# Kernel optimization log

Hardware: AMD Instinct MI355X
Metric: run time of the kernel (lower is better)

The kernel has to match this reference:

```python
import jax, jax.numpy as jnp
import numpy as np

NEG_INF = -1e9  # module uses -1e9 negativeInfinity constant
BS, DA, SL, H = 16, 512, 1024, 8


def setup_inputs() -> dict:
    key = jax.random.key(0)
    ks = jax.random.split(key, 8)
    return {
        "q":    jax.random.normal(ks[0], (BS, DA, SL), dtype=jnp.float32),
        "k_in": jax.random.normal(ks[1], (BS, DA, SL), dtype=jnp.float32),
        "v_in": jax.random.normal(ks[2], (BS, DA, SL), dtype=jnp.float32),
        "k_w":  jax.random.normal(ks[3], (DA, DA), dtype=jnp.float32) * 0.05,
        "k_b":  jax.random.normal(ks[4], (DA,), dtype=jnp.float32) * 0.05,
        "v_w":  jax.random.normal(ks[5], (DA, DA), dtype=jnp.float32) * 0.05,
        "v_b":  jax.random.normal(ks[6], (DA,), dtype=jnp.float32) * 0.05,
        "gbn_gamma": jnp.ones((H,), dtype=jnp.float32),
        "gbn_bias":  jnp.zeros((H,), dtype=jnp.float32),
        "gbn_m":     jnp.zeros((H,), dtype=jnp.float32),
        "gbn_s":     jnp.ones((H,), dtype=jnp.float32),
        "mask": jax.random.randint(ks[7], (BS, 1, 1, SL), 0, 2, dtype=jnp.int32),
    }


def reference(q, k_in, v_in, k_w, k_b, v_w, v_b, gbn_gamma, gbn_bias, gbn_m, gbn_s, mask):
    bs, da, qsl = q.shape
    h = gbn_gamma.shape[0]
    dh = da // h
    sl = k_in.shape[2]
    mask_b = mask.astype(bool)                 # [bs,1,1,sl] True = masked

    # 1x1 conv1d projections == per-position matmul over channels
    k = jnp.einsum('ok,bks->bos', k_w, k_in) + k_b[None, :, None]   # [bs,da,sl]
    v = jnp.einsum('ov,bvs->bos', v_w, v_in) + v_b[None, :, None]   # [bs,dva,sl]
    dva = v.shape[1]
    dvh = dva // h

    qh = q.reshape(bs, h, dh, qsl).transpose(0, 1, 3, 2)   # [bs,h,qsl,dh]
    kh = k.reshape(bs, h, dh, sl)                          # [bs,h,dh,sl]
    vh = v.reshape(bs, h, dvh, sl).transpose(0, 1, 3, 2)   # [bs,h,sl,dvh]

    scores = jnp.einsum('bhqd,bhds->bhqs', qh, kh)         # [bs,h,qsl,sl]

    # GhostBatchNorm1d(features=h) in eval mode: per-head affine normalization
    scores = (scores - gbn_m[None, :, None, None]) / gbn_s[None, :, None, None]
    scores = scores * gbn_gamma[None, :, None, None] + gbn_bias[None, :, None, None]

    mask_k = mask_b                           # [bs,1,1,sl]  mask key positions (selfAttention fill)
    mask_q = jnp.swapaxes(mask_b, 2, 3)       # [bs,1,sl,1]  mask query rows (transposed fill)
    scores = jnp.where(mask_k, NEG_INF, scores)
    scores = jnp.where(mask_q, NEG_INF, scores)

    w = jax.nn.softmax(scores, axis=-1)
    w = jnp.where(mask_q, 0.0, w)             # v_weights.masked_fill(mask, 0)

    out = jnp.einsum('bhqs,bhsd->bhqd', w, vh)             # [bs,h,qsl,dvh]
    out = out.transpose(0, 1, 3, 2).reshape(bs, dva, qsl)  # back to channels-first
    return out
```

## Files before the change

kernel.cpp:

```cpp
#include <hip/hip_runtime.h>

typedef _Float16 f16;
typedef _Float16 h8_t __attribute__((ext_vector_type(8)));
typedef _Float16 h4_t __attribute__((ext_vector_type(4)));
typedef float f32x4 __attribute__((ext_vector_type(4)));
typedef float f32x16 __attribute__((ext_vector_type(16)));

#define BS 16
#define DA 512
#define SL 1024
#define NH 8
#define DH 64

__device__ __forceinline__ void gload_lds16(const void* g, void* l) {
  __builtin_amdgcn_global_load_lds((const __attribute__((address_space(1))) void*)g,
                                   (__attribute__((address_space(3))) void*)l, 16, 0, 0);
}

__global__ __launch_bounds__(256) void prep_kernel(
    const float* __restrict__ k_in, const float* __restrict__ v_in,
    const float* __restrict__ k_w, const float* __restrict__ v_w,
    f16* __restrict__ Kt, f16* __restrict__ Vt,
    f16* __restrict__ kwh, f16* __restrict__ vwh) {
  const int blk = blockIdx.x;
  const int t = threadIdx.x;
  if (blk < 2048) {
    const int which = blk >> 10;
    const int r = blk & 1023;
    const int b = r >> 6;
    const int c0 = ((r >> 3) & 7) * 64;
    const int s0 = (r & 7) * 128;
    const float* src = which ? v_in : k_in;
    f16* dst = which ? Vt : Kt;
    __shared__ __align__(16) float Xf32[64 * 132];
#pragma unroll
    for (int p = 0; p < 8; ++p) {
      const int idx = p * 256 + t;
      const int cc = idx >> 5, s4 = (idx & 31) * 4;
      const float4 v = *(const float4*)&src[((size_t)b * DA + c0 + cc) * SL + s0 + s4];
      *(float4*)&Xf32[cc * 132 + s4] = v;
    }
    __syncthreads();
    const int srow = t >> 1, cb = (t & 1) * 32;
#pragma unroll
    for (int g = 0; g < 4; ++g) {
      h8_t h;
#pragma unroll
      for (int u = 0; u < 8; ++u) h[u] = (f16)Xf32[(cb + g * 8 + u) * 132 + srow];
      *(h8_t*)&dst[((size_t)b * SL + s0 + srow) * DA + c0 + cb + g * 8] = h;
    }
  } else {
    const int r = blk - 2048;
    const int wsel = r >> 5;
    const float* src = wsel ? v_w : k_w;
    f16* dst = wsel ? vwh : kwh;
    const int base = (r & 31) * 8192;
#pragma unroll
    for (int p = 0; p < 4; ++p) {
      const int i = base + p * 2048 + t * 8;
      const float4 a = *(const float4*)&src[i];
      const float4 c = *(const float4*)&src[i + 4];
      h8_t h;
      h[0] = (f16)a.x; h[1] = (f16)a.y; h[2] = (f16)a.z; h[3] = (f16)a.w;
      h[4] = (f16)c.x; h[5] = (f16)c.y; h[6] = (f16)c.z; h[7] = (f16)c.w;
      *(h8_t*)&dst[i] = h;
    }
  }
}

__global__ __launch_bounds__(256, 4) void proj_gemm_all(
    const f16* __restrict__ kwh, const f16* __restrict__ vwh,
    const f16* __restrict__ Kt, const f16* __restrict__ Vt,
    const float* __restrict__ k_b, const float* __restrict__ v_b,
    f16* __restrict__ kp, f16* __restrict__ vp) {
  __shared__ __align__(16) f16 LD[2][8192];
  const int mode = blockIdx.z;
  const int b = blockIdx.y;
  const int tx = blockIdx.x;
  const int m0 = (mode ? (tx >> 2) : (tx & 3)) * 128;
  const int n0 = (mode ? (tx & 3) : (tx >> 2)) * 128;
  const int t = threadIdx.x;
  const int lane = t & 63, w = t >> 6, lr = lane & 15, lq = lane >> 4;
  const int wm = (w >> 1) * 64, wn = (w & 1) * 64;

  const f16* Arow = (mode ? Vt + (size_t)b * SL * DA : kwh) + (size_t)m0 * DA;
  const f16* Brow = (mode ? vwh : Kt + (size_t)b * SL * DA) + (size_t)n0 * DA;

  const int rr = t >> 2;
  const int c8 = (t & 3) * 8;
  const int lo8 = t * 8;

  const f16* ga0 = Arow + (size_t)rr * DA + c8;
  const f16* ga1 = Arow + (size_t)(64 + rr) * DA + c8;
  const f16* gb0 = Brow + (size_t)rr * DA + c8;
  const f16* gb1 = Brow + (size_t)(64 + rr) * DA + c8;

  f32x4 acc[4][4] = {};

  gload_lds16(ga0, &LD[0][0] + lo8);
  gload_lds16(ga1, &LD[0][2048] + lo8);
  gload_lds16(gb0, &LD[0][4096] + lo8);
  gload_lds16(gb1, &LD[0][6144] + lo8);
  ga0 += 32; ga1 += 32; gb0 += 32; gb1 += 32;

  for (int kt = 0; kt < 16; ++kt) {
    const int cur = kt & 1;
    if (kt < 15) {
      f16* nb = &LD[cur ^ 1][0];
      gload_lds16(ga0, nb + lo8);
      gload_lds16(ga1, nb + 2048 + lo8);
      gload_lds16(gb0, nb + 4096 + lo8);
      gload_lds16(gb1, nb + 6144 + lo8);
      ga0 += 32; ga1 += 32; gb0 += 32; gb1 += 32;
      asm volatile("s_waitcnt vmcnt(4)" ::: "memory");
    } else {
      asm volatile("s_waitcnt vmcnt(0)" ::: "memory");
    }
    __builtin_amdgcn_s_barrier();
    __builtin_amdgcn_sched_barrier(0);

    const f16* Al = &LD[cur][0];
    const f16* Bl = &LD[cur][4096];
    h8_t af[4], bf[4];
#pragma unroll
    for (int i = 0; i < 4; ++i) af[i] = *(const h8_t*)&Al[(wm + i * 16 + lr) * 32 + lq * 8];
#pragma unroll
    for (int j = 0; j < 4; ++j) bf[j] = *(const h8_t*)&Bl[(wn + j * 16 + lr) * 32 + lq * 8];
    __builtin_amdgcn_s_setprio(1);
#pragma unroll
    for (int i = 0; i < 4; ++i)
#pragma unroll
      for (int j = 0; j < 4; ++j)
        acc[i][j] = __builtin_amdgcn_mfma_f32_16x16x32_f16(af[i], bf[j], acc[i][j], 0, 0, 0);
    __builtin_amdgcn_s_setprio(0);

    if (kt < 15) {
      __builtin_amdgcn_sched_barrier(0);
      __builtin_amdgcn_s_barrier();
      __builtin_amdgcn_sched_barrier(0);
    }
  }

#pragma unroll
  for (int i = 0; i < 4; ++i) {
    const int gmb = m0 + wm + i * 16 + lq * 4;
    float bm[4] = {0.f, 0.f, 0.f, 0.f};
    if (mode == 0) {
      const float4 b4 = *(const float4*)&k_b[gmb];
      bm[0] = b4.x; bm[1] = b4.y; bm[2] = b4.z; bm[3] = b4.w;
    }
#pragma unroll
    for (int j = 0; j < 4; ++j) {
      const int gn = n0 + wn + j * 16 + lr;
      const float bn = mode ? v_b[gn] : 0.f;
      h4_t hv;
#pragma unroll
      for (int r = 0; r < 4; ++r) {
        const float val = acc[i][j][r] + (mode == 0 ? bm[r] : bn);
        hv[r] = (f16)val;
      }
      f16* dst = mode ? &vp[((size_t)b * DA + gn) * SL + gmb]
                      : &kp[((size_t)b * SL + gn) * DA + gmb];
      *(h4_t*)dst = hv;
    }
  }
}

template <int MODE>
__global__ __launch_bounds__(256) void fused_proj(const float* __restrict__ Wg,
                                                  const float* __restrict__ Xin,
                                                  const float* __restrict__ bias,
                                                  f16* __restrict__ outg) {
  constexpr int MT = MODE ? SL : DA;
  constexpr int NT = MODE ? DA : SL;
  __shared__ f16 Wl[128 * 40];
  __shared__ f16 Xl[128 * 40];
  __shared__ float Xf32[32 * 132];
  const int b = blockIdx.z;
  const int m0 = blockIdx.x * 128;
  const int n0 = blockIdx.y * 128;
  const int o_base = MODE ? n0 : m0;
  const int s_base = MODE ? m0 : n0;
  const int t = threadIdx.x;
  const int w = t >> 6, lane = t & 63, lr = lane & 15, lq = lane >> 4;
  const int wm = (w >> 1) * 64, wn = (w & 1) * 64;

  f32x4 acc[4][4] = {};

  for (int kt = 0; kt < 16; ++kt) {
    const int c0 = kt * 32;
    __syncthreads();
#pragma unroll
    for (int p = 0; p < 4; ++p) {
      const int idx = p * 256 + t;
      const int row = idx >> 3, cq = (idx & 7) * 4;
      const float4 v = *(const float4*)&Wg[(size_t)(o_base + row) * DA + c0 + cq];
      h4_t hv;
      hv[0] = (f16)v.x; hv[1] = (f16)v.y; hv[2] = (f16)v.z; hv[3] = (f16)v.w;
      *(h4_t*)&Wl[row * 40 + cq] = hv;
    }
#pragma unroll
    for (int p = 0; p < 4; ++p) {
      const int idx = p * 256 + t;
      const int cc = idx >> 5, s4 = (idx & 31) * 4;
      const float4 v = *(const float4*)&Xin[((size_t)b * DA + c0 + cc) * SL + s_base + s4];
      *(float4*)&Xf32[cc * 132 + s4] = v;
    }
    __syncthreads();
    {
      const int srow = t >> 1, cb = (t & 1) * 16;
      h8_t lo, hi;
#pragma unroll
      for (int u = 0; u < 8; ++u) lo[u] = (f16)Xf32[(cb + u) * 132 + srow];
#pragma unroll
      for (int u = 0; u < 8; ++u) hi[u] = (f16)Xf32[(cb + 8 + u) * 132 + srow];
      *(h8_t*)&Xl[srow * 40 + cb] = lo;
      *(h8_t*)&Xl[srow * 40 + cb + 8] = hi;
    }
    __syncthreads();
    const f16* Alp = MODE ? Xl : Wl;
    const f16* Blp = MODE ? Wl : Xl;
    h8_t af[4], bf[4];
#pragma unroll
    for (int i = 0; i < 4; ++i) af[i] = *(const h8_t*)&Alp[(wm + i * 16 + lr) * 40 + lq * 8];
#pragma unroll
    for (int j = 0; j < 4; ++j) bf[j] = *(const h8_t*)&Blp[(wn + j * 16 + lr) * 40 + lq * 8];
#pragma unroll
    for (int i = 0; i < 4; ++i)
#pragma unroll
      for (int j = 0; j < 4; ++j)
        acc[i][j] = __builtin_amdgcn_mfma_f32_16x16x32_f16(af[i], bf[j], acc[i][j], 0, 0, 0);
  }

#pragma unroll
  for (int i = 0; i < 4; ++i) {
    const int gmb = m0 + wm + i * 16 + lq * 4;
    float bm[4] = {0.f, 0.f, 0.f, 0.f};
    if (MODE == 0) {
      const float4 b4 = *(const float4*)&bias[gmb];
      bm[0] = b4.x; bm[1] = b4.y; bm[2] = b4.z; bm[3] = b4.w;
    }
#pragma unroll
    for (int j = 0; j < 4; ++j) {
      const int gn = n0 + wn + j * 16 + lr;
      const float bn = (MODE == 1) ? bias[gn] : 0.f;
      h4_t hv;
#pragma unroll
      for (int r = 0; r < 4; ++r) {
        const float val = acc[i][j][r] + (MODE == 0 ? bm[r] : bn);
        hv[r] = (f16)val;
      }
      *(h4_t*)&outg[((size_t)b * NT + gn) * MT + gmb] = hv;
    }
  }
}

__global__ __launch_bounds__(512, 4) void attn_kernel(
    const float* __restrict__ qg, const f16* __restrict__ kp, const f16* __restrict__ vp,
    const float* __restrict__ gamma, const float* __restrict__ gbns,
    const int* __restrict__ maskg, float* __restrict__ outg) {
  __shared__ __align__(16) char smem[36864];
  f16* KV = (f16*)smem;
  float* Osh = (float*)smem;

  const int bh = blockIdx.x, b = bh >> 3, h = bh & 7;
  const int i0 = blockIdx.y * 256;
  const int t = threadIdx.x, w = t >> 6, lane = t & 63;
  const int l5 = lane & 31, hf = lane >> 5;
  const float scale = gamma[h] / gbns[h] * 1.44269504088896f;
  const int iw = i0 + w * 32 + l5;

  h8_t qf[4];
#pragma unroll
  for (int ks = 0; ks < 4; ++ks) {
    h8_t v;
#pragma unroll
    for (int u = 0; u < 8; ++u) {
      const int d = ks * 16 + hf * 8 + u;
      v[u] = (f16)(qg[((size_t)b * DA + h * DH + d) * SL + iw] * scale);
    }
    qf[ks] = v;
  }
  h8_t qf5;
#pragma unroll
  for (int u = 0; u < 8; ++u) qf5[u] = (f16)0.f;
  if (hf == 0) qf5[0] = (f16)1.f;

  const int srow = t >> 3;
  const int c8 = (t & 7) * 8;

  uint4 rk = *(const uint4*)&kp[((size_t)b * SL + srow) * DA + h * DH + c8];
  uint4 rv = *(const uint4*)&vp[((size_t)b * DA + h * DH + srow) * SL + c8];
  int mbn = maskg[b * SL + srow];

  if (t < 128) {
    const int zr = t & 63, zb = t >> 6;
    uint4 z; z.x = 0; z.y = 0; z.z = 0; z.w = 0;
    *(uint4*)&KV[zb * 9216 + zr * 72 + 64] = z;
  }
  __syncthreads();
  {
    f16* K0 = KV;
    f16* V0 = KV + 4608;
    const int rowp = (srow & ~12) | ((srow & 4) << 1) | ((srow & 8) >> 1);
    *(uint4*)&K0[rowp * 72 + c8] = rk;
    *(uint4*)&V0[srow * 72 + c8] = rv;
    if ((t & 7) == 0) K0[rowp * 72 + 64] = mbn ? (f16)(-30000.f) : (f16)0.f;
  }
  __syncthreads();

  float m_i = -3e38f, l_i = 0.f;
  f32x16 acc[2] = {};

  for (int jt = 0; jt < 16; ++jt) {
    const int j0 = jt * 64;
    const f16* Kc = KV + (jt & 1) * 9216;
    const f16* Vc = Kc + 4608;

    if (jt < 15) {
      const int jn = j0 + 64;
      rk = *(const uint4*)&kp[((size_t)b * SL + jn + srow) * DA + h * DH + c8];
      rv = *(const uint4*)&vp[((size_t)b * DA + h * DH + srow) * SL + jn + c8];
      mbn = maskg[b * SL + jn + srow];
    }

    f32x16 sa[2] = {};
    __builtin_amdgcn_s_setprio(1);
#pragma unroll
    for (int ks = 0; ks < 4; ++ks)
#pragma unroll
      for (int mj = 0; mj < 2; ++mj) {
        const h8_t kf = *(const h8_t*)&Kc[(mj * 32 + l5) * 72 + ks * 16 + hf * 8];
        sa[mj] = __builtin_amdgcn_mfma_f32_32x32x16_f16(kf, qf[ks], sa[mj], 0, 0, 0);
      }
#pragma unroll
    for (int mj = 0; mj < 2; ++mj) {
      const h8_t kf5 = *(const h8_t*)&Kc[(mj * 32 + l5) * 72 + 64];
      sa[mj] = __builtin_amdgcn_mfma_f32_32x32x16_f16(kf5, qf5, sa[mj], 0, 0, 0);
    }
    __builtin_amdgcn_s_setprio(0);

    {
      float a[8];
#pragma unroll
      for (int u = 0; u < 8; ++u)
        a[u] = fmaxf(fmaxf(sa[0][u], sa[0][u + 8]), fmaxf(sa[1][u], sa[1][u + 8]));
      float mx = fmaxf(fmaxf(fmaxf(a[0], a[1]), fmaxf(a[2], a[3])),
                       fmaxf(fmaxf(a[4], a[5]), fmaxf(a[6], a[7])));
      mx = fmaxf(mx, __shfl_xor(mx, 32));
      if (!__all(mx - m_i <= 8.0f)) {
        const float mn = fmaxf(m_i, mx);
        const float alpha = __builtin_amdgcn_exp2f(m_i - mn);
        m_i = mn;
        l_i *= alpha;
#pragma unroll
        for (int nd = 0; nd < 2; ++nd)
#pragma unroll
          for (int e = 0; e < 16; ++e) acc[nd][e] *= alpha;
      }
    }

    float r0 = 0.f, r1 = 0.f, r2 = 0.f, r3 = 0.f;
    __builtin_amdgcn_s_setprio(1);
#pragma unroll
    for (int jk = 0; jk < 4; ++jk) {
      const int mj = jk >> 1, g = jk & 1;
      float p0 = __builtin_amdgcn_exp2f(sa[mj][g * 8 + 0] - m_i);
      float p1 = __builtin_amdgcn_exp2f(sa[mj][g * 8 + 1] - m_i);
      float p2 = __builtin_amdgcn_exp2f(sa[mj][g * 8 + 2] - m_i);
      float p3 = __builtin_amdgcn_exp2f(sa[mj][g * 8 + 3] - m_i);
      float p4 = __builtin_amdgcn_exp2f(sa[mj][g * 8 + 4] - m_i);
      float p5 = __builtin_amdgcn_exp2f(sa[mj][g * 8 + 5] - m_i);
      float p6 = __builtin_amdgcn_exp2f(sa[mj][g * 8 + 6] - m_i);
      float p7 = __builtin_amdgcn_exp2f(sa[mj][g * 8 + 7] - m_i);
      h8_t pk;
      pk[0] = (f16)p0; pk[1] = (f16)p1; pk[2] = (f16)p2; pk[3] = (f16)p3;
      pk[4] = (f16)p4; pk[5] = (f16)p5; pk[6] = (f16)p6; pk[7] = (f16)p7;
      r0 += p0 + p4; r1 += p1 + p5; r2 += p2 + p6; r3 += p3 + p7;
#pragma unroll
      for (int nd = 0; nd < 2; ++nd) {
        const h8_t vf = *(const h8_t*)&Vc[(nd * 32 + l5) * 72 + jk * 16 + hf * 8];
        acc[nd] = __builtin_amdgcn_mfma_f32_32x32x16_f16(vf, pk, acc[nd], 0, 0, 0);
      }
    }
    __builtin_amdgcn_s_setprio(0);
    {
      float rs = (r0 + r1) + (r2 + r3);
      rs += __shfl_xor(rs, 32);
      l_i += rs;
    }

    if (jt < 15) {
      f16* Kn = KV + ((jt + 1) & 1) * 9216;
      f16* Vn = Kn + 4608;
      const int rowp = (srow & ~12) | ((srow & 4) << 1) | ((srow & 8) >> 1);
      *(uint4*)&Kn[rowp * 72 + c8] = rk;
      *(uint4*)&Vn[srow * 72 + c8] = rv;
      if ((t & 7) == 0) Kn[rowp * 72 + 64] = mbn ? (f16)(-30000.f) : (f16)0.f;
      __syncthreads();
    }
  }

  const int mo = maskg[b * SL + iw];
  const float fac = mo ? 0.f : 1.f / l_i;
  __syncthreads();

#pragma unroll
  for (int nd = 0; nd < 2; ++nd) {
#pragma unroll
    for (int e = 0; e < 16; ++e) {
      const int dl = (e & 3) + 8 * (e >> 2) + 4 * hf;
      Osh[dl * 256 + w * 32 + l5] = acc[nd][e] * fac;
    }
    __syncthreads();
#pragma unroll
    for (int pass = 0; pass < 4; ++pass) {
      const int row = pass * 8 + (t >> 6);
      const int i4 = (t & 63) * 4;
      const float4 o = *(const float4*)&Osh[row * 256 + i4];
      *(float4*)&outg[((size_t)b * DA + h * DH + nd * 32 + row) * SL + i0 + i4] = o;
    }
    __syncthreads();
  }
}

extern "C" void kernel_launch(void* const* d_in, const int* in_sizes, int n_in,
                              void* d_out, int out_size, void* d_ws, size_t ws_size,
                              hipStream_t stream) {
  const float* q     = (const float*)d_in[0];
  const float* k_in  = (const float*)d_in[1];
  const float* v_in  = (const float*)d_in[2];
  const float* k_w   = (const float*)d_in[3];
  const float* k_b   = (const float*)d_in[4];
  const float* v_w   = (const float*)d_in[5];
  const float* v_b   = (const float*)d_in[6];
  const float* gamma = (const float*)d_in[7];
  const float* gbns  = (const float*)d_in[10];
  const int*   mask  = (const int*)d_in[11];
  float* out = (float*)d_out;

  const size_t NEL = (size_t)BS * SL * DA;
  f16* kpw = (f16*)d_ws;
  f16* vpw = kpw + NEL;

  const size_t need = NEL * 2 * 4 + (size_t)DA * DA * 2 * 2;
  if (ws_size >= need) {
    f16* Kt  = vpw + NEL;
    f16* Vt  = Kt + NEL;
    f16* kwh = Vt + NEL;
    f16* vwh = kwh + (size_t)DA * DA;
    prep_kernel<<<dim3(2112), 256, 0, stream>>>(k_in, v_in, k_w, v_w, Kt, Vt, kwh, vwh);
    proj_gemm_all<<<dim3(32, BS, 2), 256, 0, stream>>>(kwh, vwh, Kt, Vt, k_b, v_b, kpw, vpw);
  } else {
    fused_proj<0><<<dim3(4, 8, BS), 256, 0, stream>>>(k_w, k_in, k_b, kpw);
    fused_proj<1><<<dim3(8, 4, BS), 256, 0, stream>>>(v_w, v_in, v_b, vpw);
  }
  attn_kernel<<<dim3(BS * NH, SL / 256), 512, 0, stream>>>(q, kpw, vpw, gamma, gbns, mask, out);
}
```

Measured before the change: 236.8 us.

## Split attention key range across two blocks and merge with a combine kernel

Adds a split-K (flash-decoding style) attention path: each block handles half of the key tiles and writes normalized partial outputs plus per-row max/sum, and a new combine kernel rescales and merges the two halves. This doubles the grid (512 to 1024 blocks) to raise occupancy and CU utilization, and raises launch bounds to 8 waves per CU. The cost is an extra kernel launch, extra global traffic for partial outputs, and an fp16 rounding of the second partial. The original single-pass kernel remains only for the small-workspace fallback.

New measurement: 865.2 us. 265% more time.

```diff
diff --git a/kernel.cpp b/kernel.cpp
--- a/kernel.cpp
+++ b/kernel.cpp
@@ -255,16 +255,19 @@
   }
 }
 
-__global__ __launch_bounds__(512, 4) void attn_kernel(
+__global__ __launch_bounds__(512, 8) void attn_part(
     const float* __restrict__ qg, const f16* __restrict__ kp, const f16* __restrict__ vp,
     const float* __restrict__ gamma, const float* __restrict__ gbns,
-    const int* __restrict__ maskg, float* __restrict__ outg) {
+    const int* __restrict__ maskg,
+    float* __restrict__ oA, f16* __restrict__ oB, float2* __restrict__ ml) {
   __shared__ __align__(16) char smem[36864];
   f16* KV = (f16*)smem;
   float* Osh = (float*)smem;
 
   const int bh = blockIdx.x, b = bh >> 3, h = bh & 7;
   const int i0 = blockIdx.y * 256;
+  const int jh = blockIdx.z;
+  const int jt0 = jh * 8;
   const int t = threadIdx.x, w = t >> 6, lane = t & 63;
   const int l5 = lane & 31, hf = lane >> 5;
   const float scale = gamma[h] / gbns[h] * 1.44269504088896f;
@@ -289,9 +292,9 @@
   const int srow = t >> 3;
   const int c8 = (t & 7) * 8;
 
-  uint4 rk = *(const uint4*)&kp[((size_t)b * SL + srow) * DA + h * DH + c8];
-  uint4 rv = *(const uint4*)&vp[((size_t)b * DA + h * DH + srow) * SL + c8];
-  int mbn = maskg[b * SL + srow];
+  uint4 rk = *(const uint4*)&kp[((size_t)b * SL + jt0 * 64 + srow) * DA + h * DH + c8];
+  uint4 rv = *(const uint4*)&vp[((size_t)b * DA + h * DH + srow) * SL + jt0 * 64 + c8];
+  int mbn = maskg[b * SL + jt0 * 64 + srow];
 
   if (t < 128) {
     const int zr = t & 63, zb = t >> 6;
@@ -312,12 +315,12 @@
   float m_i = -3e38f, l_i = 0.f;
   f32x16 acc[2] = {};
 
-  for (int jt = 0; jt < 16; ++jt) {
+  for (int jt = jt0; jt < jt0 + 8; ++jt) {
     const int j0 = jt * 64;
     const f16* Kc = KV + (jt & 1) * 9216;
     const f16* Vc = Kc + 4608;
 
-    if (jt < 15) {
+    if (jt < jt0 + 7) {
       const int jn = j0 + 64;
       rk = *(const uint4*)&kp[((size_t)b * SL + jn + srow) * DA + h * DH + c8];
       rv = *(const uint4*)&vp[((size_t)b * DA + h * DH + srow) * SL + jn + c8];
@@ -390,6 +393,223 @@
       l_i += rs;
     }
 
+    if (jt < jt0 + 7) {
+      f16* Kn = KV + ((jt + 1) & 1) * 9216;
+      f16* Vn = Kn + 4608;
+      const int rowp = (srow & ~12) | ((srow & 4) << 1) | ((srow & 8) >> 1);
+      *(uint4*)&Kn[rowp * 72 + c8] = rk;
+      *(uint4*)&Vn[srow * 72 + c8] = rv;
+      if ((t & 7) == 0) Kn[rowp * 72 + 64] = mbn ? (f16)(-30000.f) : (f16)0.f;
+      __syncthreads();
+    }
+  }
+
+  const float fac = 1.f / l_i;
+  if (hf == 0) {
+    float2 v; v.x = m_i; v.y = l_i;
+    ml[(size_t)jh * (128 * 1024) + (size_t)bh * 1024 + iw] = v;
+  }
+  __syncthreads();
+
+#pragma unroll
+  for (int nd = 0; nd < 2; ++nd) {
+#pragma unroll
+    for (int e = 0; e < 16; ++e) {
+      const int dl = (e & 3) + 8 * (e >> 2) + 4 * hf;
+      Osh[dl * 256 + w * 32 + l5] = acc[nd][e] * fac;
+    }
+    __syncthreads();
+#pragma unroll
+    for (int pass = 0; pass < 4; ++pass) {
+      const int row = pass * 8 + (t >> 6);
+      const int i4 = (t & 63) * 4;
+      const float4 o = *(const float4*)&Osh[row * 256 + i4];
+      const size_t off = ((size_t)bh * 64 + nd * 32 + row) * SL + i0 + i4;
+      if (jh == 0) {
+        *(float4*)&oA[off] = o;
+      } else {
+        h4_t hv;
+        hv[0] = (f16)o.x; hv[1] = (f16)o.y; hv[2] = (f16)o.z; hv[3] = (f16)o.w;
+        *(h4_t*)&oB[off] = hv;
+      }
+    }
+    __syncthreads();
+  }
+}
+
+__global__ __launch_bounds__(256) void attn_combine(
+    const f16* __restrict__ oB, const float2* __restrict__ ml,
+    const int* __restrict__ maskg, float* __restrict__ out) {
+  const int blk = blockIdx.x;
+  const int bh = blk >> 2, b = bh >> 3;
+  const int ic = (blk & 3) * 256;
+  const int t = threadIdx.x;
+  const int i = ic + (t & 63) * 4;
+  const int d0 = t >> 6;
+
+  float wA[4], wB[4];
+  const int4 m4 = *(const int4*)&maskg[b * SL + i];
+  const int mo[4] = {m4.x, m4.y, m4.z, m4.w};
+#pragma unroll
+  for (int u = 0; u < 4; ++u) {
+    const float2 a = ml[(size_t)bh * 1024 + i + u];
+    const float2 bb = ml[(size_t)128 * 1024 + (size_t)bh * 1024 + i + u];
+    const float mT = fmaxf(a.x, bb.x);
+    const float eA = __builtin_amdgcn_exp2f(a.x - mT) * a.y;
+    const float eB = __builtin_amdgcn_exp2f(bb.x - mT) * bb.y;
+    const float inv = 1.f / (eA + eB);
+    wA[u] = mo[u] ? 0.f : eA * inv;
+    wB[u] = mo[u] ? 0.f : eB * inv;
+  }
+#pragma unroll
+  for (int r = 0; r < 16; ++r) {
+    const int d = r * 4 + d0;
+    const size_t off = ((size_t)bh * 64 + d) * SL + i;
+    float4 o = *(const float4*)&out[off];
+    const h4_t b4 = *(const h4_t*)&oB[off];
+    o.x = wA[0] * o.x + wB[0] * (float)b4[0];
+    o.y = wA[1] * o.y + wB[1] * (float)b4[1];
+    o.z = wA[2] * o.z + wB[2] * (float)b4[2];
+    o.w = wA[3] * o.w + wB[3] * (float)b4[3];
+    *(float4*)&out[off] = o;
+  }
+}
+
+__global__ __launch_bounds__(512, 4) void attn_kernel(
+    const float* __restrict__ qg, const f16* __restrict__ kp, const f16* __restrict__ vp,
+    const float* __restrict__ gamma, const float* __restrict__ gbns,
+    const int* __restrict__ maskg, float* __restrict__ outg) {
+  __shared__ __align__(16) char smem[36864];
+  f16* KV = (f16*)smem;
+  float* Osh = (float*)smem;
+
+  const int bh = blockIdx.x, b = bh >> 3, h = bh & 7;
+  const int i0 = blockIdx.y * 256;
+  const int t = threadIdx.x, w = t >> 6, lane = t & 63;
+  const int l5 = lane & 31, hf = lane >> 5;
+  const float scale = gamma[h] / gbns[h] * 1.44269504088896f;
+  const int iw = i0 + w * 32 + l5;
+
+  h8_t qf[4];
+#pragma unroll
+  for (int ks = 0; ks < 4; ++ks) {
+    h8_t v;
+#pragma unroll
+    for (int u = 0; u < 8; ++u) {
+      const int d = ks * 16 + hf * 8 + u;
+      v[u] = (f16)(qg[((size_t)b * DA + h * DH + d) * SL + iw] * scale);
+    }
+    qf[ks] = v;
+  }
+  h8_t qf5;
+#pragma unroll
+  for (int u = 0; u < 8; ++u) qf5[u] = (f16)0.f;
+  if (hf == 0) qf5[0] = (f16)1.f;
+
+  const int srow = t >> 3;
+  const int c8 = (t & 7) * 8;
+
+  uint4 rk = *(const uint4*)&kp[((size_t)b * SL + srow) * DA + h * DH + c8];
+  uint4 rv = *(const uint4*)&vp[((size_t)b * DA + h * DH + srow) * SL + c8];
+  int mbn = maskg[b * SL + srow];
+
+  if (t < 128) {
+    const int zr = t & 63, zb = t >> 6;
+    uint4 z; z.x = 0; z.y = 0; z.z = 0; z.w = 0;
+    *(uint4*)&KV[zb * 9216 + zr * 72 + 64] = z;
+  }
+  __syncthreads();
+  {
+    f16* K0 = KV;
+    f16* V0 = KV + 4608;
+    const int rowp = (srow & ~12) | ((srow & 4) << 1) | ((srow & 8) >> 1);
+    *(uint4*)&K0[rowp * 72 + c8] = rk;
+    *(uint4*)&V0[srow * 72 + c8] = rv;
+    if ((t & 7) == 0) K0[rowp * 72 + 64] = mbn ? (f16)(-30000.f) : (f16)0.f;
+  }
+  __syncthreads();
+
+  float m_i = -3e38f, l_i = 0.f;
+  f32x16 acc[2] = {};
+
+  for (int jt = 0; jt < 16; ++jt) {
+    const int j0 = jt * 64;
+    const f16* Kc = KV + (jt & 1) * 9216;
+    const f16* Vc = Kc + 4608;
+
+    if (jt < 15) {
+      const int jn = j0 + 64;
+      rk = *(const uint4*)&kp[((size_t)b * SL + jn + srow) * DA + h * DH + c8];
+      rv = *(const uint4*)&vp[((size_t)b * DA + h * DH + srow) * SL + jn + c8];
+      mbn = maskg[b * SL + jn + srow];
+    }
+
+    f32x16 sa[2] = {};
+    __builtin_amdgcn_s_setprio(1);
+#pragma unroll
+    for (int ks = 0; ks < 4; ++ks)
+#pragma unroll
+      for (int mj = 0; mj < 2; ++mj) {
+        const h8_t kf = *(const h8_t*)&Kc[(mj * 32 + l5) * 72 + ks * 16 + hf * 8];
+        sa[mj] = __builtin_amdgcn_mfma_f32_32x32x16_f16(kf, qf[ks], sa[mj], 0, 0, 0);
+      }
+#pragma unroll
+    for (int mj = 0; mj < 2; ++mj) {
+      const h8_t kf5 = *(const h8_t*)&Kc[(mj * 32 + l5) * 72 + 64];
+      sa[mj] = __builtin_amdgcn_mfma_f32_32x32x16_f16(kf5, qf5, sa[mj], 0, 0, 0);
+    }
+    __builtin_amdgcn_s_setprio(0);
+
+    {
+      float a[8];
+#pragma unroll
+      for (int u = 0; u < 8; ++u)
+        a[u] = fmaxf(fmaxf(sa[0][u], sa[0][u + 8]), fmaxf(sa[1][u], sa[1][u + 8]));
+      float mx = fmaxf(fmaxf(fmaxf(a[0], a[1]), fmaxf(a[2], a[3])),
+                       fmaxf(fmaxf(a[4], a[5]), fmaxf(a[6], a[7])));
+      mx = fmaxf(mx, __shfl_xor(mx, 32));
+      if (!__all(mx - m_i <= 8.0f)) {
+        const float mn = fmaxf(m_i, mx);
+        const float alpha = __builtin_amdgcn_exp2f(m_i - mn);
+        m_i = mn;
+        l_i *= alpha;
+#pragma unroll
+        for (int nd = 0; nd < 2; ++nd)
+#pragma unroll
+          for (int e = 0; e < 16; ++e) acc[nd][e] *= alpha;
+      }
+    }
+
+    float r0 = 0.f, r1 = 0.f, r2 = 0.f, r3 = 0.f;
+    __builtin_amdgcn_s_setprio(1);
+#pragma unroll
+    for (int jk = 0; jk < 4; ++jk) {
+      const int mj = jk >> 1, g = jk & 1;
+      float p0 = __builtin_amdgcn_exp2f(sa[mj][g * 8 + 0] - m_i);
+      float p1 = __builtin_amdgcn_exp2f(sa[mj][g * 8 + 1] - m_i);
+      float p2 = __builtin_amdgcn_exp2f(sa[mj][g * 8 + 2] - m_i);
+      float p3 = __builtin_amdgcn_exp2f(sa[mj][g * 8 + 3] - m_i);
+      float p4 = __builtin_amdgcn_exp2f(sa[mj][g * 8 + 4] - m_i);
+      float p5 = __builtin_amdgcn_exp2f(sa[mj][g * 8 + 5] - m_i);
+      float p6 = __builtin_amdgcn_exp2f(sa[mj][g * 8 + 6] - m_i);
+      float p7 = __builtin_amdgcn_exp2f(sa[mj][g * 8 + 7] - m_i);
+      h8_t pk;
+      pk[0] = (f16)p0; pk[1] = (f16)p1; pk[2] = (f16)p2; pk[3] = (f16)p3;
+      pk[4] = (f16)p4; pk[5] = (f16)p5; pk[6] = (f16)p6; pk[7] = (f16)p7;
+      r0 += p0 + p4; r1 += p1 + p5; r2 += p2 + p6; r3 += p3 + p7;
+#pragma unroll
+      for (int nd = 0; nd < 2; ++nd) {
+        const h8_t vf = *(const h8_t*)&Vc[(nd * 32 + l5) * 72 + jk * 16 + hf * 8];
+        acc[nd] = __builtin_amdgcn_mfma_f32_32x32x16_f16(vf, pk, acc[nd], 0, 0, 0);
+      }
+    }
+    __builtin_amdgcn_s_setprio(0);
+    {
+      float rs = (r0 + r1) + (r2 + r3);
+      rs += __shfl_xor(rs, 32);
+      l_i += rs;
+    }
+
     if (jt < 15) {
       f16* Kn = KV + ((jt + 1) & 1) * 9216;
       f16* Vn = Kn + 4608;
@@ -451,9 +671,14 @@
     f16* vwh = kwh + (size_t)DA * DA;
     prep_kernel<<<dim3(2112), 256, 0, stream>>>(k_in, v_in, k_w, v_w, Kt, Vt, kwh, vwh);
     proj_gemm_all<<<dim3(32, BS, 2), 256, 0, stream>>>(kwh, vwh, Kt, Vt, k_b, v_b, kpw, vpw);
+    f16* oB = Kt;
+    float2* ml = (float2*)Vt;
+    attn_part<<<dim3(BS * NH, SL / 256, 2), 512, 0, stream>>>(
+        q, kpw, vpw, gamma, gbns, mask, out, oB, ml);
+    attn_combine<<<dim3(512), 256, 0, stream>>>(oB, ml, mask, out);
   } else {
     fused_proj<0><<<dim3(4, 8, BS), 256, 0, stream>>>(k_w, k_in, k_b, kpw);
     fused_proj<1><<<dim3(8, 4, BS), 256, 0, stream>>>(v_w, v_in, v_b, vpw);
-  }
-  attn_kernel<<<dim3(BS * NH, SL / 256), 512, 0, stream>>>(q, kpw, vpw, gamma, gbns, mask, out);
-}
+    attn_kernel<<<dim3(BS * NH, SL / 256), 512, 0, stream>>>(q, kpw, vpw, gamma, gbns, mask, out);
+  }
+}
```
